# Optimization experiments

Measured on AMD Instinct MI355X. Metric: run time of the kernel, lower is better.

Reference implementation:

```python
import jax, jax.numpy as jnp
import numpy as np

D_MODEL = 192
D_INNER = 384   # expand=2
D_STATE = 16
D_CONV = 4
DT_RANK = 12    # ceil(192/16)
DEPTH = 4
STRIDE = 4
N_PATCH = 400   # 1600 // 4
NCLS = 1000
BATCH = 32
EPS = 1e-5


def setup_inputs() -> dict:
    key = jax.random.key(0)
    ks = iter(jax.random.split(key, 64))
    nrm = lambda shp, s=0.02: jax.random.normal(next(ks), shp, jnp.float32) * s
    inp = {}
    inp["imgs"] = jax.random.normal(next(ks), (BATCH, 1, 40, 40), jnp.float32)
    # StrideEmbed: conv1d(kernel=stride=4) == per-patch linear on [B,400,4]
    inp["patch_w"] = nrm((STRIDE, D_MODEL))
    inp["patch_b"] = jnp.zeros((D_MODEL,), jnp.float32)
    inp["cls_token"] = nrm((1, 1, D_MODEL))
    inp["pos_embed"] = nrm((1, N_PATCH + 1, D_MODEL))
    # per-block Mamba params, stacked on a leading depth axis
    inp["norm_ws"] = jnp.ones((DEPTH, D_MODEL), jnp.float32)
    inp["in_proj_ws"] = nrm((DEPTH, D_MODEL, 2 * D_INNER))
    inp["conv_ws"] = nrm((DEPTH, D_INNER, D_CONV), 0.2)
    inp["conv_bs"] = jnp.zeros((DEPTH, D_INNER), jnp.float32)
    inp["x_proj_ws"] = nrm((DEPTH, D_INNER, DT_RANK + 2 * D_STATE))
    inp["dt_proj_ws"] = nrm((DEPTH, DT_RANK, D_INNER), 0.1)
    # dt bias ~ inverse-softplus of small positive dt
    inp["dt_proj_bs"] = jnp.log(jnp.expm1(jnp.full((DEPTH, D_INNER), 0.01, jnp.float32)))
    inp["A_logs"] = jnp.log(jnp.broadcast_to(
        jnp.arange(1, D_STATE + 1, dtype=jnp.float32), (DEPTH, D_INNER, D_STATE)))
    inp["Ds"] = jnp.ones((DEPTH, D_INNER), jnp.float32)
    inp["out_proj_ws"] = nrm((DEPTH, D_INNER, D_MODEL))
    inp["norm_f_w"] = jnp.ones((D_MODEL,), jnp.float32)
    inp["head_w"] = nrm((D_MODEL, NCLS))
    inp["head_b"] = jnp.zeros((NCLS,), jnp.float32)
    return inp


def rmsnorm(x, w):
    return x * jax.lax.rsqrt(jnp.mean(x * x, axis=-1, keepdims=True) + EPS) * w


def mamba_mixer(x, in_w, conv_w, conv_b, xp_w, dt_w, dt_b, A_log, Dp, out_w):
    # x: [B, L, D_MODEL]
    B, L, _ = x.shape
    xz = x @ in_w                         # [B, L, 2*d_inner]
    u, z = jnp.split(xz, 2, axis=-1)
    # causal depthwise conv1d (kernel 4), truncated to L, then SiLU
    upad = jnp.pad(u, ((0, 0), (D_CONV - 1, 0), (0, 0)))
    uc = sum(upad[:, k:k + L, :] * conv_w[:, k] for k in range(D_CONV)) + conv_b
    uc = jax.nn.silu(uc)
    # input-dependent dt, B, C
    dbl = uc @ xp_w                       # [B, L, dt_rank + 2*d_state]
    dt = dbl[..., :DT_RANK]
    Bm = dbl[..., DT_RANK:DT_RANK + D_STATE]
    Cm = dbl[..., DT_RANK + D_STATE:]
    delta = jax.nn.softplus(dt @ dt_w + dt_b)           # [B, L, d_inner]
    A = -jnp.exp(A_log)                                  # [d_inner, d_state]
    dA = jnp.exp(delta[..., None] * A)                   # [B, L, d_inner, d_state]
    dBu = (delta * uc)[..., None] * Bm[:, :, None, :]    # [B, L, d_inner, d_state]

    def step(h, t):
        da, dbu, c = t
        h = da * h + dbu                                 # [B, d_inner, d_state]
        y = jnp.einsum('bds,bs->bd', h, c)
        return h, y

    h0 = jnp.zeros((B, D_INNER, D_STATE), x.dtype)
    _, ys = jax.lax.scan(step, h0, (jnp.moveaxis(dA, 1, 0),
                                    jnp.moveaxis(dBu, 1, 0),
                                    jnp.moveaxis(Cm, 1, 0)))
    y = jnp.moveaxis(ys, 0, 1) + uc * Dp                 # [B, L, d_inner]
    return (y * jax.nn.silu(z)) @ out_w


def reference(imgs, patch_w, patch_b, cls_token, pos_embed, norm_ws, in_proj_ws,
              conv_ws, conv_bs, x_proj_ws, dt_proj_ws, dt_proj_bs, A_logs, Ds,
              out_proj_ws, norm_f_w, head_w, head_b):
    B = imgs.shape[0]
    seq = imgs.reshape(B, N_PATCH, STRIDE)               # [B, 400, 4] (in_chans=1)
    x = seq @ patch_w + patch_b + pos_embed[:, :-1, :]   # patch embed + pos (cls pos is last)
    cls = cls_token + pos_embed[:, -1:, :]
    x = jnp.concatenate([x, jnp.broadcast_to(cls, (B, 1, D_MODEL))], axis=1)  # cls appended at end
    residual = None
    for i in range(DEPTH):
        residual = x if residual is None else x + residual  # fused add-norm, prenorm
        h = rmsnorm(residual, norm_ws[i])
        x = mamba_mixer(h, in_proj_ws[i], conv_ws[i], conv_bs[i], x_proj_ws[i],
                        dt_proj_ws[i], dt_proj_bs[i], A_logs[i], Ds[i], out_proj_ws[i])
    x = rmsnorm(x + residual, norm_f_w)                   # final fused add-norm, prenorm=False
    return x[:, -1, :] @ head_w + head_b                  # head on cls (last) token
```

## Files before the change

kernel.cpp:

```cpp
#include <hip/hip_runtime.h>
#include <hip/hip_bf16.h>
#include <hip/hip_fp16.h>

using bf16 = __hip_bfloat16;
typedef short short8 __attribute__((ext_vector_type(8)));
typedef float floatx4 __attribute__((ext_vector_type(4)));

#define LSEQ 401
#define NTOK 12832
#define NTOKP 12864
#define DM 192
#define DI 384
#define NB 32
#define NCH 13
#define CHT 32

#define O_IMGS   0
#define O_PW     51200
#define O_PB     51968
#define O_CLS    52160
#define O_POS    52352
#define O_NORMW  129344
#define O_INW    130112
#define O_CONVW  719936
#define O_CONVB  726080
#define O_XPW    727616
#define O_DTW    795200
#define O_DTB    813632
#define O_ALOG   815168
#define O_DS     839744
#define O_OUTW   841280
#define O_NORMF  1136192
#define O_HEADW  1136384
#define O_HEADB  1328384
#define WTOT     1329408

#define BO_INWT  0
#define BO_XPWT  589824
#define BO_OUTWT 688128
#define BFTOT_F  491520

__constant__ int g_sz[18] = {51200, 768, 192, 192, 76992, 768, 589824, 6144, 1536,
                             67584, 18432, 1536, 24576, 1536, 294912, 192, 192000, 1000};
__constant__ int g_off[18] = {O_IMGS, O_PW, O_PB, O_CLS, O_POS, O_NORMW, O_INW, O_CONVW,
                              O_CONVB, O_XPW, O_DTW, O_DTB, O_ALOG, O_DS, O_OUTW,
                              O_NORMF, O_HEADW, O_HEADB};

struct SrcPtrs { const void* p[18]; };

static __device__ __forceinline__ int probe_flag(const unsigned short* probe) {
    unsigned short u0 = probe[0];
    if (u0 == 0x3F80u) return 0;
    if (u0 == 0x3C00u) return 2;
    return 1;
}
static __device__ __forceinline__ float load_src(int flag, const void* p, long i) {
    if (flag == 0) return __bfloat162float(((const bf16*)p)[i]);
    if (flag == 2) return __half2float(((const __half*)p)[i]);
    return ((const float*)p)[i];
}
static __device__ __forceinline__ unsigned short f2b(float f) {
    bf16 h = __float2bfloat16(f);
    return *reinterpret_cast<unsigned short*>(&h);
}
static __device__ __forceinline__ float b2f_us(unsigned short us) {
    unsigned int ui = (unsigned int)us << 16;
    return __uint_as_float(ui);
}

__global__ void convert_kernel(SrcPtrs sp, const unsigned short* __restrict__ probe,
                               float* __restrict__ dst) {
    int flag = probe_flag(probe);
    int which = blockIdx.y;
    int n = g_sz[which];
    const void* src = sp.p[which];
    float* d = dst + g_off[which];
    for (int i = blockIdx.x * blockDim.x + threadIdx.x; i < n; i += gridDim.x * blockDim.x)
        d[i] = load_src(flag, src, i);
}

__global__ void prep_wt_kernel(SrcPtrs sp, const unsigned short* __restrict__ probe,
                               unsigned short* __restrict__ bfw) {
    int flag = probe_flag(probe);
    int which = blockIdx.y, layer = blockIdx.z;
    int i = blockIdx.x * 256 + threadIdx.x;
    if (which == 0) {
        if (i >= 768 * 192) return;
        int n = i / 192, k = i % 192;
        float v = load_src(flag, sp.p[6], (long)layer * 147456 + (long)k * 768 + n);
        bfw[BO_INWT + (long)layer * 147456 + i] = f2b(v);
    } else if (which == 1) {
        if (i >= 64 * 384) return;
        int n = i / 384, k = i % 384;
        float v = (n < 44) ? load_src(flag, sp.p[9], (long)layer * 16896 + (long)k * 44 + n) : 0.f;
        bfw[BO_XPWT + (long)layer * 24576 + i] = f2b(v);
    } else {
        if (i >= 192 * 384) return;
        int n = i / 384, k = i % 384;
        float v = load_src(flag, sp.p[14], (long)layer * 73728 + (long)k * 192 + n);
        bfw[BO_OUTWT + (long)layer * 73728 + i] = f2b(v);
    }
}

__global__ __launch_bounds__(192) void embed_kernel(const float* __restrict__ W, float* __restrict__ x) {
    const float* imgs = W + O_IMGS;
    const float* pw   = W + O_PW;
    const float* pb   = W + O_PB;
    const float* cls  = W + O_CLS;
    const float* pos  = W + O_POS;
    int tok = blockIdx.x;
    int b = tok / LSEQ, t = tok % LSEQ;
    int c = threadIdx.x;
    float v;
    if (t < 400) {
        float s0 = imgs[b * 1600 + t * 4 + 0];
        float s1 = imgs[b * 1600 + t * 4 + 1];
        float s2 = imgs[b * 1600 + t * 4 + 2];
        float s3 = imgs[b * 1600 + t * 4 + 3];
        v = s0 * pw[0 * DM + c] + s1 * pw[1 * DM + c] +
            s2 * pw[2 * DM + c] + s3 * pw[3 * DM + c] + pb[c] + pos[t * DM + c];
    } else {
        v = cls[c] + pos[400 * DM + c];
    }
    x[(long)tok * DM + c] = v;
}

__global__ __launch_bounds__(256) void resnorm_kernel(
    const float* __restrict__ x, float* __restrict__ res, unsigned short* __restrict__ hbf,
    const float* __restrict__ w, int first) {
    int wv = threadIdx.x >> 6, lane = threadIdx.x & 63;
    long tok = (long)blockIdx.x * 4 + wv;
    long base = tok * DM + lane * 4;
    float4 v = make_float4(0.f, 0.f, 0.f, 0.f);
    bool real = (tok < NTOK);
    if (real && lane < 48) {
        v = *(const float4*)(x + base);
        if (!first) {
            float4 r = *(const float4*)(res + base);
            v.x += r.x; v.y += r.y; v.z += r.z; v.w += r.w;
        }
        *(float4*)(res + base) = v;
    }
    float ss = v.x * v.x + v.y * v.y + v.z * v.z + v.w * v.w;
#pragma unroll
    for (int o = 1; o < 64; o <<= 1) ss += __shfl_xor(ss, o, 64);
    float inv = rsqrtf(ss * (1.f / DM) + 1e-5f);
    if (lane < 48) {
        if (real) {
            float4 w4 = *(const float4*)(w + lane * 4);
            ushort4 h;
            h.x = f2b(v.x * inv * w4.x); h.y = f2b(v.y * inv * w4.y);
            h.z = f2b(v.z * inv * w4.z); h.w = f2b(v.w * inv * w4.w);
            *(ushort4*)(hbf + base) = h;
        } else if (tok < NTOKP) {
            ushort4 h; h.x = h.y = h.z = h.w = 0;
            *(ushort4*)(hbf + base) = h;
        }
    }
}

template <int OUTBF>
__global__ __launch_bounds__(256) void gemm_mfma(
    const unsigned short* __restrict__ A, const unsigned short* __restrict__ Wt,
    void* __restrict__ C, int K, int N, int NC) {
    __shared__ unsigned short sA[64][72];
    __shared__ unsigned short sW[64][72];
    int tid = threadIdx.x;
    int w = tid >> 6, lane = tid & 63;
    int q = lane >> 4, m = lane & 15;
    long tok0 = (long)blockIdx.x * 64;
    int n0 = blockIdx.y * 64;
    floatx4 acc[4] = {};
    for (int k0 = 0; k0 < K; k0 += 64) {
        int slot = tid;
#pragma unroll
        for (int i = 0; i < 2; ++i, slot += 256) {
            int r = slot >> 3, c8 = (slot & 7) * 8;
            *(short8*)&sA[r][c8] = *(const short8*)(A + (tok0 + r) * K + k0 + c8);
            *(short8*)&sW[r][c8] = *(const short8*)(Wt + (long)(n0 + r) * K + k0 + c8);
        }
        __syncthreads();
#pragma unroll
        for (int q2 = 0; q2 < 64; q2 += 32) {
            short8 bfr = *(const short8*)&sA[w * 16 + m][q2 + q * 8];
#pragma unroll
            for (int nt = 0; nt < 4; ++nt) {
                short8 afr = *(const short8*)&sW[nt * 16 + m][q2 + q * 8];
                acc[nt] = __builtin_amdgcn_mfma_f32_16x16x32_bf16(afr, bfr, acc[nt], 0, 0, 0);
            }
        }
        __syncthreads();
    }
    long tok = tok0 + w * 16 + m;
#pragma unroll
    for (int nt = 0; nt < 4; ++nt) {
        int ch = n0 + nt * 16 + q * 4;
        if (OUTBF) {
            unsigned short* dst = (unsigned short*)C + tok * NC + ch;
            ushort4 h4;
            h4.x = f2b(acc[nt][0]); h4.y = f2b(acc[nt][1]);
            h4.z = f2b(acc[nt][2]); h4.w = f2b(acc[nt][3]);
            *(ushort4*)dst = h4;
        } else {
            float* dst = (float*)C + tok * NC + ch;
            if (ch + 3 < N) {
                *(float4*)dst = make_float4(acc[nt][0], acc[nt][1], acc[nt][2], acc[nt][3]);
            } else {
#pragma unroll
                for (int r = 0; r < 4; ++r)
                    if (ch + r < N) dst[r] = acc[nt][r];
            }
        }
    }
}

__global__ __launch_bounds__(256) void gemm_xproj(
    const unsigned short* __restrict__ A, const unsigned short* __restrict__ Wt,
    float* __restrict__ dblP) {
    __shared__ unsigned short sA[64][72];
    __shared__ unsigned short sW[64][72];
    int tid = threadIdx.x;
    int w = tid >> 6, lane = tid & 63;
    int q = lane >> 4, m = lane & 15;
    long tok0 = (long)blockIdx.x * 64;
    int koff = blockIdx.y * 128;
    float* C = dblP + (long)blockIdx.y * NTOKP * 44;
    floatx4 acc[4] = {};
    for (int k0 = 0; k0 < 128; k0 += 64) {
        int slot = tid;
#pragma unroll
        for (int i = 0; i < 2; ++i, slot += 256) {
            int r = slot >> 3, c8 = (slot & 7) * 8;
            *(short8*)&sA[r][c8] = *(const short8*)(A + (tok0 + r) * DI + koff + k0 + c8);
            *(short8*)&sW[r][c8] = *(const short8*)(Wt + (long)r * DI + koff + k0 + c8);
        }
        __syncthreads();
#pragma unroll
        for (int q2 = 0; q2 < 64; q2 += 32) {
            short8 bfr = *(const short8*)&sA[w * 16 + m][q2 + q * 8];
#pragma unroll
            for (int nt = 0; nt < 4; ++nt) {
                short8 afr = *(const short8*)&sW[nt * 16 + m][q2 + q * 8];
                acc[nt] = __builtin_amdgcn_mfma_f32_16x16x32_bf16(afr, bfr, acc[nt], 0, 0, 0);
            }
        }
        __syncthreads();
    }
    long tok = tok0 + w * 16 + m;
#pragma unroll
    for (int nt = 0; nt < 4; ++nt) {
        int ch = nt * 16 + q * 4;
        float* dst = C + tok * 44 + ch;
        if (ch + 3 < 44) {
            *(float4*)dst = make_float4(acc[nt][0], acc[nt][1], acc[nt][2], acc[nt][3]);
        } else {
#pragma unroll
            for (int r = 0; r < 4; ++r)
                if (ch + r < 44) dst[r] = acc[nt][r];
        }
    }
}

__global__ __launch_bounds__(256) void dbl_sum_kernel(const float* __restrict__ dblP,
                                                      float* __restrict__ dbl) {
    int i = blockIdx.x * 256 + threadIdx.x;
    if (i < NTOK * 44)
        dbl[i] = dblP[i] + dblP[(long)NTOKP * 44 + i] + dblP[(long)2 * NTOKP * 44 + i];
}

__global__ __launch_bounds__(384) void conv_silu_kernel(
    const unsigned short* __restrict__ xzb, const float* __restrict__ cw,
    const float* __restrict__ cb, unsigned short* __restrict__ ucb) {
    int b = blockIdx.y;
    int t0 = blockIdx.x * 8;
    int d = threadIdx.x;
    float w0 = cw[d * 4 + 0], w1 = cw[d * 4 + 1], w2 = cw[d * 4 + 2], w3 = cw[d * 4 + 3];
    float bias = cb[d];
    long tb = (long)b * LSEQ;
    float uv[11];
#pragma unroll
    for (int j = 0; j < 11; ++j) {
        int t = t0 - 3 + j;
        uv[j] = (t >= 0 && t < LSEQ) ? b2f_us(xzb[(tb + t) * 768 + d]) : 0.f;
    }
#pragma unroll
    for (int j = 0; j < 8; ++j) {
        int t = t0 + j;
        if (t < LSEQ) {
            float acc = bias + w0 * uv[j] + w1 * uv[j + 1] + w2 * uv[j + 2] + w3 * uv[j + 3];
            float sv = acc / (1.f + __expf(-acc));
            ucb[(tb + t) * DI + d] = f2b(sv);
        }
    }
}

__global__ __launch_bounds__(256) void scan_sum_kernel(
    const float* __restrict__ dbl, const unsigned short* __restrict__ ucb,
    const float* __restrict__ dtw, const float* __restrict__ dtb,
    const float* __restrict__ Alog, float* __restrict__ deltaBuf,
    float* __restrict__ Aprod, float* __restrict__ Hend) {
    int ch = blockIdx.x, b = blockIdx.y;
    int tid = threadIdx.x;
    int shalf = tid & 1;
    int d = blockIdx.z * 128 + (tid >> 1);
    int t0 = ch * CHT;
    long tokb = (long)b * LSEQ + t0;
    int tmax = min(CHT, LSEQ - t0);
    bool last = (ch == NCH - 1);
    __shared__ float sdt[CHT][12];
    __shared__ float sB[CHT][16];
    for (int i = tid; i < tmax * 12; i += 256) {
        int r = i / 12, k = i % 12;
        sdt[r][k] = dbl[(tokb + r) * 44 + k];
    }
    if (!last) {
        for (int i = tid; i < CHT * 16; i += 256) {
            int r = i >> 4, s = i & 15;
            sB[r][s] = dbl[(tokb + r) * 44 + 12 + s];
        }
    }
    float dtwr[12];
#pragma unroll
    for (int k = 0; k < 12; ++k) dtwr[k] = dtw[k * DI + d];
    float bias = dtb[d];
    float a[8];
#pragma unroll
    for (int s = 0; s < 8; ++s) a[s] = -__expf(Alog[d * 16 + shalf * 8 + s]);
    float h[8] = {};
    float sumd = 0.f;
    __syncthreads();
    float u0 = b2f_us(ucb[tokb * DI + d]);
    float u1 = b2f_us(ucb[(tokb + min(1, tmax - 1)) * DI + d]);
#pragma unroll 2
    for (int t = 0; t < tmax; ++t) {
        int tp = min(t + 2, tmax - 1);
        float u2 = b2f_us(ucb[(tokb + tp) * DI + d]);
        float acc = bias;
#pragma unroll
        for (int k = 0; k < 12; ++k) acc = fmaf(sdt[t][k], dtwr[k], acc);
        float delta = (acc > 20.f) ? acc : __logf(1.f + __expf(acc));
        if (shalf == 0) deltaBuf[(tokb + t) * DI + d] = delta;
        if (!last) {
            float du = delta * u0;
            sumd += delta;
            float Bv[8];
            *(float4*)&Bv[0] = *(const float4*)&sB[t][shalf * 8];
            *(float4*)&Bv[4] = *(const float4*)&sB[t][shalf * 8 + 4];
#pragma unroll
            for (int s = 0; s < 8; ++s) {
                float da = __expf(delta * a[s]);
                h[s] = fmaf(da, h[s], du * Bv[s]);
            }
        }
        u0 = u1; u1 = u2;
    }
    if (!last) {
        long idx = (((long)b * NCH + ch) * DI + d) * 16 + shalf * 8;
        float ap[8], he[8];
#pragma unroll
        for (int s = 0; s < 8; ++s) { ap[s] = __expf(a[s] * sumd); he[s] = h[s]; }
        *(float4*)(Aprod + idx) = *(float4*)&ap[0];
        *(float4*)(Aprod + idx + 4) = *(float4*)&ap[4];
        *(float4*)(Hend + idx) = *(float4*)&he[0];
        *(float4*)(Hend + idx + 4) = *(float4*)&he[4];
    }
}

__global__ __launch_bounds__(256) void scan_combine_kernel(
    const float* __restrict__ Ap, const float* __restrict__ He, float* __restrict__ hinit) {
    long gid = (long)blockIdx.x * 256 + threadIdx.x;
    int b = (int)(gid / 6144);
    int r = (int)(gid % 6144);
    float carry = 0.f;
#pragma unroll
    for (int j = 0; j < NCH; ++j) {
        long idx = ((long)b * NCH + j) * 6144 + r;
        hinit[idx] = carry;
        if (j < NCH - 1) carry = fmaf(Ap[idx], carry, He[idx]);
    }
}

__global__ __launch_bounds__(256) void scan_main_kernel(
    const float* __restrict__ deltaBuf, const unsigned short* __restrict__ ucb,
    const unsigned short* __restrict__ xzb, const float* __restrict__ Alog,
    const float* __restrict__ Dvec, const float* __restrict__ hinit,
    const float* __restrict__ dbl, unsigned short* __restrict__ ybf) {
    int ch = blockIdx.x, b = blockIdx.y;
    int tid = threadIdx.x;
    int shalf = tid & 1;
    int d = blockIdx.z * 128 + (tid >> 1);
    int t0 = ch * CHT;
    long tokb = (long)b * LSEQ + t0;
    int tmax = min(CHT, LSEQ - t0);
    __shared__ float sB[CHT][16], sC[CHT][16];
    for (int i = tid; i < CHT * 16; i += 256) {
        int r = i >> 4, s = i & 15;
        bool ok = (r < tmax);
        sB[r][s] = ok ? dbl[(tokb + r) * 44 + 12 + s] : 0.f;
        sC[r][s] = ok ? dbl[(tokb + r) * 44 + 28 + s] : 0.f;
    }
    float a[8];
#pragma unroll
    for (int s = 0; s < 8; ++s) a[s] = -__expf(Alog[d * 16 + shalf * 8 + s]);
    float h[8];
    long hidx = (((long)b * NCH + ch) * DI + d) * 16 + shalf * 8;
    *(float4*)&h[0] = *(const float4*)(hinit + hidx);
    *(float4*)&h[4] = *(const float4*)(hinit + hidx + 4);
    float Dp = Dvec[d];
    __syncthreads();
    int t1i = min(1, tmax - 1);
    float d0 = deltaBuf[tokb * DI + d];
    float u0 = b2f_us(ucb[tokb * DI + d]);
    float z0 = b2f_us(xzb[tokb * 768 + DI + d]);
    float d1 = deltaBuf[(tokb + t1i) * DI + d];
    float u1 = b2f_us(ucb[(tokb + t1i) * DI + d]);
    float z1 = b2f_us(xzb[(tokb + t1i) * 768 + DI + d]);
#pragma unroll 2
    for (int t = 0; t < tmax; ++t) {
        int tp = min(t + 2, tmax - 1);
        float d2 = deltaBuf[(tokb + tp) * DI + d];
        float u2 = b2f_us(ucb[(tokb + tp) * DI + d]);
        float z2 = b2f_us(xzb[(tokb + tp) * 768 + DI + d]);
        float Bv[8], Cv[8];
        *(float4*)&Bv[0] = *(const float4*)&sB[t][shalf * 8];
        *(float4*)&Bv[4] = *(const float4*)&sB[t][shalf * 8 + 4];
        *(float4*)&Cv[0] = *(const float4*)&sC[t][shalf * 8];
        *(float4*)&Cv[4] = *(const float4*)&sC[t][shalf * 8 + 4];
        float du = d0 * u0;
        float y0 = 0.f, y1 = 0.f, y2 = 0.f, y3 = 0.f;
#pragma unroll
        for (int s = 0; s < 8; s += 4) {
            float da0 = __expf(d0 * a[s]);
            float da1 = __expf(d0 * a[s + 1]);
            float da2 = __expf(d0 * a[s + 2]);
            float da3 = __expf(d0 * a[s + 3]);
            h[s]     = fmaf(da0, h[s],     du * Bv[s]);
            h[s + 1] = fmaf(da1, h[s + 1], du * Bv[s + 1]);
            h[s + 2] = fmaf(da2, h[s + 2], du * Bv[s + 2]);
            h[s + 3] = fmaf(da3, h[s + 3], du * Bv[s + 3]);
            y0 = fmaf(h[s],     Cv[s],     y0);
            y1 = fmaf(h[s + 1], Cv[s + 1], y1);
            y2 = fmaf(h[s + 2], Cv[s + 2], y2);
            y3 = fmaf(h[s + 3], Cv[s + 3], y3);
        }
        float p = (y0 + y1) + (y2 + y3);
        p += __shfl_xor(p, 1, 64);
        if (shalf == 0) {
            float y = fmaf(u0, Dp, p);
            float gz = z0 / (1.f + __expf(-z0));
            ybf[(tokb + t) * DI + d] = f2b(y * gz);
        }
        d0 = d1; u0 = u1; z0 = z1;
        d1 = d2; u1 = u2; z1 = z2;
    }
}

__global__ __launch_bounds__(256) void finalnorm_kernel(
    const float* __restrict__ x, const float* __restrict__ res,
    const float* __restrict__ w, float* __restrict__ v) {
    int b = blockIdx.x;
    int c = threadIdx.x;
    long tok = (long)b * LSEQ + 400;
    __shared__ float sb[256];
    float val = 0.f;
    if (c < DM) val = x[tok * DM + c] + res[tok * DM + c];
    sb[c] = val * val;
    __syncthreads();
    for (int o = 128; o > 0; o >>= 1) {
        if (c < o) sb[c] += sb[c + o];
        __syncthreads();
    }
    float inv = rsqrtf(sb[0] * (1.f / DM) + 1e-5f);
    if (c < DM) v[b * DM + c] = val * inv * w[c];
}

__global__ __launch_bounds__(128) void head_kernel(
    const float* __restrict__ v, const float* __restrict__ hw, const float* __restrict__ hb,
    const unsigned short* __restrict__ probe, void* __restrict__ out) {
    int b = blockIdx.y;
    int n = blockIdx.x * 128 + threadIdx.x;
    __shared__ float vs[DM];
    for (int i = threadIdx.x; i < DM; i += 128) vs[i] = v[b * DM + i];
    __syncthreads();
    if (n < 1000) {
        float acc = hb[n];
#pragma unroll 4
        for (int c = 0; c < DM; ++c) acc = fmaf(vs[c], hw[c * 1000 + n], acc);
        int flag = probe_flag(probe);
        if (flag == 0)      ((bf16*)out)[b * 1000 + n] = (bf16)acc;
        else if (flag == 2) ((__half*)out)[b * 1000 + n] = __float2half(acc);
        else                ((float*)out)[b * 1000 + n] = acc;
    }
}

extern "C" void kernel_launch(void* const* d_in, const int* in_sizes, int n_in,
                              void* d_out, int out_size, void* d_ws, size_t ws_size,
                              hipStream_t stream) {
    float* ws = (float*)d_ws;
    float* Wr = ws;
    unsigned short* bfw = (unsigned short*)(ws + WTOT);
    float* act   = ws + WTOT + BFTOT_F;
    float* resT  = act;
    float* xB    = resT + (long)NTOKP * DM;
    float* dbl   = xB + (long)NTOKP * DM;
    float* dblP  = dbl + (long)NTOKP * 44;
    float* Aprod = dblP + (long)3 * NTOKP * 44;
    float* Hend  = Aprod + (long)NB * NCH * 6144;
    float* hinit = Hend + (long)NB * NCH * 6144;
    float* deltaB= hinit + (long)NB * NCH * 6144;
    float* vbuf  = deltaB + (long)NTOKP * DI;
    unsigned short* hbf = (unsigned short*)(vbuf + NB * DM);
    unsigned short* xzb = hbf + (long)NTOKP * DM;
    unsigned short* ucb = xzb + (long)NTOKP * 768;
    unsigned short* ybf = ucb + (long)NTOKP * DI;

    const unsigned short* probe = (const unsigned short*)d_in[5];

    SrcPtrs sp;
    for (int i = 0; i < 18; ++i) sp.p[i] = d_in[i];
    convert_kernel<<<dim3(64, 18), 256, 0, stream>>>(sp, probe, Wr);
    prep_wt_kernel<<<dim3(576, 3, 4), 256, 0, stream>>>(sp, probe, bfw);

    embed_kernel<<<NTOK, 192, 0, stream>>>(Wr, xB);

    for (int i = 0; i < 4; ++i) {
        resnorm_kernel<<<NTOKP / 4, 256, 0, stream>>>(xB, resT, hbf, Wr + O_NORMW + i * DM, i == 0);
        gemm_mfma<1><<<dim3(201, 12), 256, 0, stream>>>(
            hbf, bfw + BO_INWT + (long)i * 147456, xzb, 192, 768, 768);
        conv_silu_kernel<<<dim3(51, NB), 384, 0, stream>>>(
            xzb, Wr + O_CONVW + i * 1536, Wr + O_CONVB + i * DI, ucb);
        gemm_xproj<<<dim3(201, 3), 256, 0, stream>>>(
            ucb, bfw + BO_XPWT + (long)i * 24576, dblP);
        dbl_sum_kernel<<<(NTOK * 44 + 255) / 256, 256, 0, stream>>>(dblP, dbl);
        scan_sum_kernel<<<dim3(NCH, NB, 3), 256, 0, stream>>>(
            dbl, ucb, Wr + O_DTW + i * 4608, Wr + O_DTB + i * DI,
            Wr + O_ALOG + i * 6144, deltaB, Aprod, Hend);
        scan_combine_kernel<<<(NB * 6144) / 256, 256, 0, stream>>>(Aprod, Hend, hinit);
        scan_main_kernel<<<dim3(NCH, NB, 3), 256, 0, stream>>>(
            deltaB, ucb, xzb, Wr + O_ALOG + i * 6144, Wr + O_DS + i * DI,
            hinit, dbl, ybf);
        gemm_mfma<0><<<dim3(201, 3), 256, 0, stream>>>(
            ybf, bfw + BO_OUTWT + (long)i * 73728, xB, 384, 192, 192);
    }

    finalnorm_kernel<<<NB, 256, 0, stream>>>(xB, resT, Wr + O_NORMF, vbuf);
    head_kernel<<<dim3(8, NB), 128, 0, stream>>>(vbuf, Wr + O_HEADW, Wr + O_HEADB, probe, d_out);
}
```

Before: 629.5 us.

## Use 128-token GEMM tiles and fold x_proj split-K reduction into scan kernels

The generic MFMA GEMM now processes 128 tokens per block with two accumulator sets per wave, roughly halving the grid and reusing each weight tile across twice as many rows. The dedicated x_proj kernel is replaced by the generic GEMM with a z-dimension split-K of three slabs. The separate dbl_sum reduction kernel is removed, and the scan kernels sum the three partial slabs when loading dt/B/C. NTOKP is padded to a multiple of 128 so the larger tiles stay in bounds. The trade-offs are fewer blocks for occupancy and repeated partial-sum reads inside the scan kernels.

Result: no change. 639.4 us (+1.6%).

```diff
diff --git a/kernel.cpp b/kernel.cpp
--- a/kernel.cpp
+++ b/kernel.cpp
@@ -8,12 +8,13 @@
 
 #define LSEQ 401
 #define NTOK 12832
-#define NTOKP 12864
+#define NTOKP 12928
 #define DM 192
 #define DI 384
 #define NB 32
 #define NCH 13
 #define CHT 32
+#define SLAB ((long)NTOKP * 44)
 
 #define O_IMGS   0
 #define O_PW     51200
@@ -162,110 +163,70 @@
 template <int OUTBF>
 __global__ __launch_bounds__(256) void gemm_mfma(
     const unsigned short* __restrict__ A, const unsigned short* __restrict__ Wt,
-    void* __restrict__ C, int K, int N, int NC) {
-    __shared__ unsigned short sA[64][72];
+    void* __restrict__ Cv, int K, int N, int NC, int sa, int sw,
+    long zA, long zW, long zC) {
+    __shared__ unsigned short sA[128][72];
     __shared__ unsigned short sW[64][72];
+    A += (long)blockIdx.z * zA;
+    Wt += (long)blockIdx.z * zW;
     int tid = threadIdx.x;
     int w = tid >> 6, lane = tid & 63;
     int q = lane >> 4, m = lane & 15;
-    long tok0 = (long)blockIdx.x * 64;
+    long tok0 = (long)blockIdx.x * 128;
     int n0 = blockIdx.y * 64;
-    floatx4 acc[4] = {};
+    floatx4 acc[2][4] = {};
     for (int k0 = 0; k0 < K; k0 += 64) {
-        int slot = tid;
-#pragma unroll
-        for (int i = 0; i < 2; ++i, slot += 256) {
-            int r = slot >> 3, c8 = (slot & 7) * 8;
-            *(short8*)&sA[r][c8] = *(const short8*)(A + (tok0 + r) * K + k0 + c8);
-            *(short8*)&sW[r][c8] = *(const short8*)(Wt + (long)(n0 + r) * K + k0 + c8);
+#pragma unroll
+        for (int p = 0; p < 4; ++p) {
+            int idx = tid + p * 256;
+            int r = idx >> 3, c8 = (idx & 7) * 8;
+            *(short8*)&sA[r][c8] = *(const short8*)(A + (tok0 + r) * sa + k0 + c8);
+        }
+#pragma unroll
+        for (int p = 0; p < 2; ++p) {
+            int idx = tid + p * 256;
+            int r = idx >> 3, c8 = (idx & 7) * 8;
+            *(short8*)&sW[r][c8] = *(const short8*)(Wt + (long)(n0 + r) * sw + k0 + c8);
         }
         __syncthreads();
 #pragma unroll
         for (int q2 = 0; q2 < 64; q2 += 32) {
-            short8 bfr = *(const short8*)&sA[w * 16 + m][q2 + q * 8];
-#pragma unroll
-            for (int nt = 0; nt < 4; ++nt) {
-                short8 afr = *(const short8*)&sW[nt * 16 + m][q2 + q * 8];
-                acc[nt] = __builtin_amdgcn_mfma_f32_16x16x32_bf16(afr, bfr, acc[nt], 0, 0, 0);
+#pragma unroll
+            for (int tf = 0; tf < 2; ++tf) {
+                short8 bfr = *(const short8*)&sA[w * 32 + tf * 16 + m][q2 + q * 8];
+#pragma unroll
+                for (int nt = 0; nt < 4; ++nt) {
+                    short8 afr = *(const short8*)&sW[nt * 16 + m][q2 + q * 8];
+                    acc[tf][nt] = __builtin_amdgcn_mfma_f32_16x16x32_bf16(afr, bfr, acc[tf][nt], 0, 0, 0);
+                }
             }
         }
         __syncthreads();
     }
-    long tok = tok0 + w * 16 + m;
-#pragma unroll
-    for (int nt = 0; nt < 4; ++nt) {
-        int ch = n0 + nt * 16 + q * 4;
-        if (OUTBF) {
-            unsigned short* dst = (unsigned short*)C + tok * NC + ch;
-            ushort4 h4;
-            h4.x = f2b(acc[nt][0]); h4.y = f2b(acc[nt][1]);
-            h4.z = f2b(acc[nt][2]); h4.w = f2b(acc[nt][3]);
-            *(ushort4*)dst = h4;
-        } else {
-            float* dst = (float*)C + tok * NC + ch;
-            if (ch + 3 < N) {
-                *(float4*)dst = make_float4(acc[nt][0], acc[nt][1], acc[nt][2], acc[nt][3]);
+#pragma unroll
+    for (int tf = 0; tf < 2; ++tf) {
+        long tok = tok0 + w * 32 + tf * 16 + m;
+#pragma unroll
+        for (int nt = 0; nt < 4; ++nt) {
+            int ch = n0 + nt * 16 + q * 4;
+            if (OUTBF) {
+                unsigned short* dst = (unsigned short*)Cv + (long)blockIdx.z * zC + tok * NC + ch;
+                ushort4 h4;
+                h4.x = f2b(acc[tf][nt][0]); h4.y = f2b(acc[tf][nt][1]);
+                h4.z = f2b(acc[tf][nt][2]); h4.w = f2b(acc[tf][nt][3]);
+                *(ushort4*)dst = h4;
             } else {
-#pragma unroll
-                for (int r = 0; r < 4; ++r)
-                    if (ch + r < N) dst[r] = acc[nt][r];
+                float* dst = (float*)Cv + (long)blockIdx.z * zC + tok * NC + ch;
+                if (ch + 3 < N) {
+                    *(float4*)dst = make_float4(acc[tf][nt][0], acc[tf][nt][1], acc[tf][nt][2], acc[tf][nt][3]);
+                } else {
+#pragma unroll
+                    for (int r = 0; r < 4; ++r)
+                        if (ch + r < N) dst[r] = acc[tf][nt][r];
+                }
             }
         }
     }
-}
-
-__global__ __launch_bounds__(256) void gemm_xproj(
-    const unsigned short* __restrict__ A, const unsigned short* __restrict__ Wt,
-    float* __restrict__ dblP) {
-    __shared__ unsigned short sA[64][72];
-    __shared__ unsigned short sW[64][72];
-    int tid = threadIdx.x;
-    int w = tid >> 6, lane = tid & 63;
-    int q = lane >> 4, m = lane & 15;
-    long tok0 = (long)blockIdx.x * 64;
-    int koff = blockIdx.y * 128;
-    float* C = dblP + (long)blockIdx.y * NTOKP * 44;
-    floatx4 acc[4] = {};
-    for (int k0 = 0; k0 < 128; k0 += 64) {
-        int slot = tid;
-#pragma unroll
-        for (int i = 0; i < 2; ++i, slot += 256) {
-            int r = slot >> 3, c8 = (slot & 7) * 8;
-            *(short8*)&sA[r][c8] = *(const short8*)(A + (tok0 + r) * DI + koff + k0 + c8);
-            *(short8*)&sW[r][c8] = *(const short8*)(Wt + (long)r * DI + koff + k0 + c8);
-        }
-        __syncthreads();
-#pragma unroll
-        for (int q2 = 0; q2 < 64; q2 += 32) {
-            short8 bfr = *(const short8*)&sA[w * 16 + m][q2 + q * 8];
-#pragma unroll
-            for (int nt = 0; nt < 4; ++nt) {
-                short8 afr = *(const short8*)&sW[nt * 16 + m][q2 + q * 8];
-                acc[nt] = __builtin_amdgcn_mfma_f32_16x16x32_bf16(afr, bfr, acc[nt], 0, 0, 0);
-            }
-        }
-        __syncthreads();
-    }
-    long tok = tok0 + w * 16 + m;
-#pragma unroll
-    for (int nt = 0; nt < 4; ++nt) {
-        int ch = nt * 16 + q * 4;
-        float* dst = C + tok * 44 + ch;
-        if (ch + 3 < 44) {
-            *(float4*)dst = make_float4(acc[nt][0], acc[nt][1], acc[nt][2], acc[nt][3]);
-        } else {
-#pragma unroll
-            for (int r = 0; r < 4; ++r)
-                if (ch + r < 44) dst[r] = acc[nt][r];
-        }
-    }
-}
-
-__global__ __launch_bounds__(256) void dbl_sum_kernel(const float* __restrict__ dblP,
-                                                      float* __restrict__ dbl) {
-    int i = blockIdx.x * 256 + threadIdx.x;
-    if (i < NTOK * 44)
-        dbl[i] = dblP[i] + dblP[(long)NTOKP * 44 + i] + dblP[(long)2 * NTOKP * 44 + i];
 }
 
 __global__ __launch_bounds__(384) void conv_silu_kernel(
@@ -295,7 +256,7 @@
 }
 
 __global__ __launch_bounds__(256) void scan_sum_kernel(
-    const float* __restrict__ dbl, const unsigned short* __restrict__ ucb,
+    const float* __restrict__ dblP, const unsigned short* __restrict__ ucb,
     const float* __restrict__ dtw, const float* __restrict__ dtb,
     const float* __restrict__ Alog, float* __restrict__ deltaBuf,
     float* __restrict__ Aprod, float* __restrict__ Hend) {
@@ -311,12 +272,14 @@
     __shared__ float sB[CHT][16];
     for (int i = tid; i < tmax * 12; i += 256) {
         int r = i / 12, k = i % 12;
-        sdt[r][k] = dbl[(tokb + r) * 44 + k];
+        long o = (tokb + r) * 44 + k;
+        sdt[r][k] = dblP[o] + dblP[o + SLAB] + dblP[o + 2 * SLAB];
     }
     if (!last) {
         for (int i = tid; i < CHT * 16; i += 256) {
             int r = i >> 4, s = i & 15;
-            sB[r][s] = dbl[(tokb + r) * 44 + 12 + s];
+            long o = (tokb + r) * 44 + 12 + s;
+            sB[r][s] = dblP[o] + dblP[o + SLAB] + dblP[o + 2 * SLAB];
         }
     }
     float dtwr[12];
@@ -384,7 +347,7 @@
     const float* __restrict__ deltaBuf, const unsigned short* __restrict__ ucb,
     const unsigned short* __restrict__ xzb, const float* __restrict__ Alog,
     const float* __restrict__ Dvec, const float* __restrict__ hinit,
-    const float* __restrict__ dbl, unsigned short* __restrict__ ybf) {
+    const float* __restrict__ dblP, unsigned short* __restrict__ ybf) {
     int ch = blockIdx.x, b = blockIdx.y;
     int tid = threadIdx.x;
     int shalf = tid & 1;
@@ -395,9 +358,13 @@
     __shared__ float sB[CHT][16], sC[CHT][16];
     for (int i = tid; i < CHT * 16; i += 256) {
         int r = i >> 4, s = i & 15;
-        bool ok = (r < tmax);
-        sB[r][s] = ok ? dbl[(tokb + r) * 44 + 12 + s] : 0.f;
-        sC[r][s] = ok ? dbl[(tokb + r) * 44 + 28 + s] : 0.f;
+        if (r < tmax) {
+            long o = (tokb + r) * 44 + 12 + s;
+            sB[r][s] = dblP[o] + dblP[o + SLAB] + dblP[o + 2 * SLAB];
+            sC[r][s] = dblP[o + 16] + dblP[o + 16 + SLAB] + dblP[o + 16 + 2 * SLAB];
+        } else {
+            sB[r][s] = 0.f; sC[r][s] = 0.f;
+        }
     }
     float a[8];
 #pragma unroll
@@ -502,9 +469,8 @@
     float* act   = ws + WTOT + BFTOT_F;
     float* resT  = act;
     float* xB    = resT + (long)NTOKP * DM;
-    float* dbl   = xB + (long)NTOKP * DM;
-    float* dblP  = dbl + (long)NTOKP * 44;
-    float* Aprod = dblP + (long)3 * NTOKP * 44;
+    float* dblP  = xB + (long)NTOKP * DM;
+    float* Aprod = dblP + 3 * SLAB;
     float* Hend  = Aprod + (long)NB * NCH * 6144;
     float* hinit = Hend + (long)NB * NCH * 6144;
     float* deltaB= hinit + (long)NB * NCH * 6144;
@@ -525,22 +491,21 @@
 
     for (int i = 0; i < 4; ++i) {
         resnorm_kernel<<<NTOKP / 4, 256, 0, stream>>>(xB, resT, hbf, Wr + O_NORMW + i * DM, i == 0);
-        gemm_mfma<1><<<dim3(201, 12), 256, 0, stream>>>(
-            hbf, bfw + BO_INWT + (long)i * 147456, xzb, 192, 768, 768);
+        gemm_mfma<1><<<dim3(101, 12), 256, 0, stream>>>(
+            hbf, bfw + BO_INWT + (long)i * 147456, xzb, 192, 768, 768, 192, 192, 0, 0, 0);
         conv_silu_kernel<<<dim3(51, NB), 384, 0, stream>>>(
             xzb, Wr + O_CONVW + i * 1536, Wr + O_CONVB + i * DI, ucb);
-        gemm_xproj<<<dim3(201, 3), 256, 0, stream>>>(
-            ucb, bfw + BO_XPWT + (long)i * 24576, dblP);
-        dbl_sum_kernel<<<(NTOK * 44 + 255) / 256, 256, 0, stream>>>(dblP, dbl);
+        gemm_mfma<0><<<dim3(101, 1, 3), 256, 0, stream>>>(
+            ucb, bfw + BO_XPWT + (long)i * 24576, dblP, 128, 44, 44, 384, 384, 128, 128, SLAB);
         scan_sum_kernel<<<dim3(NCH, NB, 3), 256, 0, stream>>>(
-            dbl, ucb, Wr + O_DTW + i * 4608, Wr + O_DTB + i * DI,
+            dblP, ucb, Wr + O_DTW + i * 4608, Wr + O_DTB + i * DI,
             Wr + O_ALOG + i * 6144, deltaB, Aprod, Hend);
         scan_combine_kernel<<<(NB * 6144) / 256, 256, 0, stream>>>(Aprod, Hend, hinit);
         scan_main_kernel<<<dim3(NCH, NB, 3), 256, 0, stream>>>(
             deltaB, ucb, xzb, Wr + O_ALOG + i * 6144, Wr + O_DS + i * DI,
-            hinit, dbl, ybf);
-        gemm_mfma<0><<<dim3(201, 3), 256, 0, stream>>>(
-            ybf, bfw + BO_OUTWT + (long)i * 73728, xB, 384, 192, 192);
+            hinit, dblP, ybf);
+        gemm_mfma<0><<<dim3(101, 3), 256, 0, stream>>>(
+            ybf, bfw + BO_OUTWT + (long)i * 73728, xB, 384, 192, 192, 384, 384, 0, 0, 0);
     }
 
     finalnorm_kernel<<<NB, 256, 0, stream>>>(xB, resT, Wr + O_NORMF, vbuf);
```
